# Optimization experiments

Hardware: AMD Instinct MI355X
Metric: run time of the kernel (lower is better)

The kernel has to match this reference:

```python
import jax, jax.numpy as jnp
import numpy as np

# Grid config from FPVNet.__init__ defaults
XB = (-50.0, 50.0, 0.5)   # xbound
YB = (-50.0, 50.0, 0.5)   # ybound
ZB = (-2.0, 6.0, 1.0)     # zbound
DB = (1.0, 50.0)          # dbound
NX, NY, NZ = 200, 200, 8


def setup_inputs() -> dict:
    key = jax.random.key(0)
    k1, k2 = jax.random.split(key)
    B, C, H, W = 8, 5, 256, 704
    # metric depth in valid range [dmin, dmax]
    depth = jax.random.uniform(k1, (B, 1, H, W), dtype=jnp.float32,
                               minval=DB[0], maxval=DB[1])
    sem_logits = jax.random.normal(k2, (B, C, H, W), dtype=jnp.float32)
    fx, fy, cx, cy = 600.0, 600.0, W / 2.0, H / 2.0
    K = jnp.tile(jnp.array([[fx, 0.0, cx], [0.0, fy, cy], [0.0, 0.0, 1.0]],
                           dtype=jnp.float32), (B, 1, 1))
    return {"depth": depth, "sem_logits": sem_logits, "K": K}


def reference(depth, sem_logits, K):
    """FPVNet._project_to_voxel: unproject pixels via intrinsics and
    scatter-add softmaxed semantics into a (B, C, nZ, nX, nY) voxel grid."""
    B, C, H, W = sem_logits.shape
    dmin, dmax = DB

    u = jnp.arange(W, dtype=jnp.float32)
    v = jnp.arange(H, dtype=jnp.float32)
    vv, uu = jnp.meshgrid(v, u, indexing='ij')            # (H, W)

    fx = K[:, 0, 0][:, None, None]
    fy = K[:, 1, 1][:, None, None]
    cx = K[:, 0, 2][:, None, None]
    cy = K[:, 1, 2][:, None, None]

    d = jnp.clip(depth[:, 0], dmin, dmax)                  # (B, H, W)
    x_cam = (uu[None] - cx) * d / fx
    y_cam = (vv[None] - cy) * d / fy
    z_cam = d

    # .astype(int) truncates toward zero, matching torch .long()
    xi = ((x_cam - XB[0]) / XB[2]).astype(jnp.int32)
    yi = ((z_cam - YB[0]) / YB[2]).astype(jnp.int32)
    zi = ((y_cam - ZB[0]) / ZB[2]).astype(jnp.int32)

    valid = ((xi >= 0) & (xi < NX) & (yi >= 0) & (yi < NY)
             & (zi >= 0) & (zi < NZ))                      # (B, H, W)

    sem_prob = jax.nn.softmax(sem_logits, axis=1)          # (B, C, H, W)

    V = NZ * NX * NY
    flat_idx = jnp.clip(zi * (NX * NY) + xi * NY + yi, 0, V - 1)
    flat_idx = flat_idx.reshape(B, -1)                     # (B, N), N = H*W
    # zero-out invalid points so clamped indices contribute nothing
    w = jnp.where(valid.reshape(B, 1, -1), sem_prob.reshape(B, C, -1), 0.0)

    def scatter_one(idx, prob):                            # idx (N,), prob (C, N)
        return jnp.zeros((C, V), dtype=prob.dtype).at[:, idx].add(prob)

    voxel = jax.vmap(scatter_one)(flat_idx, w)             # (B, C, V)
    return voxel.reshape(B, C, NZ, NX, NY)
```

## Files before the change

### kernel.cpp

```cpp
#include <hip/hip_runtime.h>

#define HH 256
#define WW 704
#define BB 8
#define CC 5
#define NXc 200
#define NYc 200
#define NZc 8
#define VV (NZc * NXc * NYc)
#define HW (HH * WW)

#define NBIN 98
#define NSUB (NBIN * 4)
#define NBKT (BB * NSUB)
#define CAP  768
#define QSTRIDE 1280

#define CUR_OFF 0
#define A_OFF   4096
#define B_OFF   (A_OFF + NBKT * CAP * 4)
#define CMP_OFF (B_OFF + NBKT * CAP * 2)
#define WS_FLOATS (CMP_OFF + NBKT * QSTRIDE)

__device__ __forceinline__ void bin_fp(int yi, int& xlo, int& xhi,
                                       int& zlo, int& zhi) {
    const float dhi   = 0.5f * (float)(yi + 1) - 50.0f;
    const float xspan = 2.0f * (352.0f / 600.0f) * dhi;
    const float zspan = (128.0f / 600.0f) * dhi;
    xlo = max(0,       (int)(100.0f - xspan) - 1);
    xhi = min(NXc - 1, (int)(100.0f + xspan) + 1);
    zlo = max(0,       (int)(2.0f - zspan) - 1);
    zhi = min(NZc - 1, (int)(2.0f + zspan) + 1);
}

__global__ __launch_bounds__(1024) void p1_scatter(
    const float* __restrict__ depth,
    const float* __restrict__ sem,
    const float* __restrict__ Kmat,
    unsigned* __restrict__ ws)
{
    __shared__ unsigned cnt[NSUB];
    __shared__ unsigned base[NSUB];

    unsigned* cursors = ws + CUR_OFF;
    float4*   arrA    = (float4*)(ws + A_OFF);
    float2*   arrB    = (float2*)(ws + B_OFF);

    const int b     = blockIdx.x & 7;
    const int inner = blockIdx.x >> 3;
    const int t     = inner * 1024 + threadIdx.x;
    const int p0    = t * 4;

    for (int i = threadIdx.x; i < NSUB; i += 1024) cnt[i] = 0;
    __syncthreads();

    const float fx = Kmat[b * 9 + 0];
    const float fy = Kmat[b * 9 + 4];
    const float cx = Kmat[b * 9 + 2];
    const float cy = Kmat[b * 9 + 5];

    const float4 d4 = *reinterpret_cast<const float4*>(depth + (size_t)b * HW + p0);
    float4 l4[CC];
#pragma unroll
    for (int c = 0; c < CC; ++c)
        l4[c] = *reinterpret_cast<const float4*>(sem + ((size_t)b * CC + c) * HW + p0);
    const float dvals[4] = {d4.x, d4.y, d4.z, d4.w};

    int      sub_r[4];
    unsigned meta_r[4];
    float    prob_r[4][CC];

#pragma unroll
    for (int j = 0; j < 4; ++j) {
        const int p = p0 + j;
        const int v = p / WW;
        const int u = p - v * WW;

        float d = fminf(fmaxf(dvals[j], 1.0f), 50.0f);
        float x_cam = ((float)u - cx) * d / fx;
        float y_cam = ((float)v - cy) * d / fy;
        int xi = (int)((x_cam + 50.0f) / 0.5f);
        int yi = (int)((d     + 50.0f) / 0.5f);
        int zi = (int)((y_cam +  2.0f) / 1.0f);

        bool valid = (xi >= 0) && (xi < NXc) && (yi >= 0) && (yi < NYc)
                  && (zi >= 0) && (zi < NZc);
        if (valid) {
            float lg[CC];
#pragma unroll
            for (int c = 0; c < CC; ++c) lg[c] = ((const float*)&l4[c])[j];
            float m = lg[0];
#pragma unroll
            for (int c = 1; c < CC; ++c) m = fmaxf(m, lg[c]);
            float s = 0.0f;
#pragma unroll
            for (int c = 0; c < CC; ++c) { prob_r[j][c] = expf(lg[c] - m); s += prob_r[j][c]; }
            const float inv_s = 1.0f / s;
#pragma unroll
            for (int c = 0; c < CC; ++c) prob_r[j][c] *= inv_s;

            const int bin = yi - 102;
            sub_r[j]  = bin * 4 + (zi & 1) * 2 + (xi >= 100 ? 1 : 0);
            meta_r[j] = (unsigned)xi | ((unsigned)zi << 8);
            atomicAdd(&cnt[sub_r[j]], 1u);
        } else {
            sub_r[j] = -1;
        }
    }
    __syncthreads();

    if (threadIdx.x < NSUB) {
        unsigned c = cnt[threadIdx.x];
        base[threadIdx.x] = c ? atomicAdd(&cursors[b * NSUB + threadIdx.x], c) : 0u;
    }
    __syncthreads();
    if (threadIdx.x < NSUB) cnt[threadIdx.x] = 0;
    __syncthreads();

#pragma unroll
    for (int j = 0; j < 4; ++j) {
        const int sub = sub_r[j];
        if (sub < 0) continue;
        unsigned r   = atomicAdd(&cnt[sub], 1u);
        unsigned off = base[sub] + r;
        if (off >= CAP) continue;
        size_t slot = (size_t)(b * NSUB + sub) * CAP + off;
        float4 ra;
        ((unsigned*)&ra)[0] = meta_r[j];
        ra.y = prob_r[j][0];  ra.z = prob_r[j][1];  ra.w = prob_r[j][2];
        arrA[slot] = ra;
        arrB[slot] = make_float2(prob_r[j][3], prob_r[j][4]);
    }
}

__global__ __launch_bounds__(256) void p2_reduce(unsigned* __restrict__ ws)
{
    const int wg  = blockIdx.x;
    const int b   = wg / NSUB;
    const int rem = wg - b * NSUB;
    const int bin = rem >> 2;
    const int q   = rem & 3;
    const int zp  = q >> 1;
    const int xh  = q & 1;
    const int yi  = 102 + bin;

    int xlo, xhi, zlo, zhi;
    bin_fp(yi, xlo, xhi, zlo, zhi);
    const int sxlo  = xh ? 100 : xlo;
    const int snx   = xh ? (xhi - 99) : (100 - xlo);
    const int zlo_p = zlo + (((zlo & 1) != zp) ? 1 : 0);
    const int nzs   = (zhi >= zlo_p) ? ((zhi - zlo_p) >> 1) + 1 : 0;
    const int cells = nzs * snx * CC;

    __shared__ float acc[4 * QSTRIDE];
    for (int i = threadIdx.x; i < 4 * cells; i += 256) acc[i] = 0.0f;
    __syncthreads();

    unsigned n = ws[CUR_OFF + wg];
    if (n > CAP) n = CAP;
    const float4* arrA = (const float4*)(ws + A_OFF);
    const float2* arrB = (const float2*)(ws + B_OFF);
    const size_t  seg  = (size_t)wg * CAP;
    const int     rep  = (threadIdx.x & 3) * cells;

    for (unsigned i = threadIdx.x; i < n; i += 256) {
        const float4 ra = arrA[seg + i];
        const float2 rb = arrB[seg + i];
        const unsigned m = ((const unsigned*)&ra)[0];
        const int xi = (int)(m & 255u);
        const int zi = (int)((m >> 8) & 15u);
        if (xi < sxlo || zi < zlo_p || zi > zhi || ((zi & 1) != zp))
            continue;
        const int ix = xi - sxlo;
        if (ix >= snx) continue;
        float* ac = acc + rep + (((zi - zlo_p) >> 1) * snx + ix) * CC;
        atomicAdd(ac + 0, ra.y);
        atomicAdd(ac + 1, ra.z);
        atomicAdd(ac + 2, ra.w);
        atomicAdd(ac + 3, rb.x);
        atomicAdd(ac + 4, rb.y);
    }
    __syncthreads();

    float* cmp = (float*)ws + CMP_OFF + (size_t)wg * QSTRIDE;
    for (int i = threadIdx.x; i < cells; i += 256)
        cmp[i] = acc[i] + acc[cells + i] + acc[2 * cells + i] + acc[3 * cells + i];
}

#define GY 20
__global__ __launch_bounds__(256) void p3_assemble(
    const float* __restrict__ wsf, float* __restrict__ out)
{
    const int id    = blockIdx.x;
    const int chunk = id & 31;
    const int gb    = id >> 5;
    const int g     = gb % 10;
    const int b     = gb / 10;
    const int t     = chunk * 256 + threadIdx.x;
    const bool live = (t < CC * NZc * NXc);

    int x = 0, z = 0, c = 0;
    if (live) { x = t % NXc; int zc = t / NXc; z = zc & 7; c = zc >> 3; }
    const int y0 = g * GY;

    __shared__ float tile[GY][256];

    for (int j = 0; j < GY; ++j) {
        float val = 0.0f;
        const int y   = y0 + j;
        const int bin = y - 102;
        if (live && bin >= 0) {
            int xlo, xhi, zlo, zhi;
            bin_fp(y, xlo, xhi, zlo, zhi);
            if (x >= xlo && x <= xhi && z >= zlo && z <= zhi) {
                const int zp    = z & 1;
                const int xh    = (x >= 100) ? 1 : 0;
                const int zlo_p = zlo + (((zlo & 1) != zp) ? 1 : 0);
                const int sxlo  = xh ? 100 : xlo;
                const int snx   = xh ? (xhi - 99) : (100 - xlo);
                const int wg    = ((b * NBIN + bin) << 2) + zp * 2 + xh;
                val = wsf[CMP_OFF + (size_t)wg * QSTRIDE
                          + (((z - zlo_p) >> 1) * snx + (x - sxlo)) * CC + c];
            }
        }
        tile[j][threadIdx.x] = val;
    }
    __syncthreads();

    if (live) {
        float* dst = out + (size_t)b * CC * VV + (size_t)t * NYc + y0;
#pragma unroll
        for (int k = 0; k < 5; ++k) {
            float4 v;
            v.x = tile[k * 4 + 0][threadIdx.x];
            v.y = tile[k * 4 + 1][threadIdx.x];
            v.z = tile[k * 4 + 2][threadIdx.x];
            v.w = tile[k * 4 + 3][threadIdx.x];
            reinterpret_cast<float4*>(dst)[k] = v;
        }
    }
}

__global__ __launch_bounds__(256) void zero_f4(float4* __restrict__ p, int n4) {
    int i = blockIdx.x * blockDim.x + threadIdx.x;
    const int stride = gridDim.x * blockDim.x;
    const float4 z = make_float4(0.f, 0.f, 0.f, 0.f);
    for (; i < n4; i += stride) p[i] = z;
}

__global__ __launch_bounds__(256) void fpv_scatter_direct(
    const float* __restrict__ depth, const float* __restrict__ sem,
    const float* __restrict__ Kmat, float* __restrict__ out)
{
    const int b  = blockIdx.x & 7;
    const int t  = (blockIdx.x >> 3) * blockDim.x + threadIdx.x;
    const int p0 = t * 4;

    const float fx = Kmat[b * 9 + 0];
    const float fy = Kmat[b * 9 + 4];
    const float cx = Kmat[b * 9 + 2];
    const float cy = Kmat[b * 9 + 5];

    const float4 d4 = *reinterpret_cast<const float4*>(depth + (size_t)b * HW + p0);
    float4 l4[CC];
#pragma unroll
    for (int c = 0; c < CC; ++c)
        l4[c] = *reinterpret_cast<const float4*>(sem + ((size_t)b * CC + c) * HW + p0);
    const float dvals[4] = {d4.x, d4.y, d4.z, d4.w};

#pragma unroll
    for (int j = 0; j < 4; ++j) {
        const int p = p0 + j;
        const int v = p / WW;
        const int u = p - v * WW;
        float d = fminf(fmaxf(dvals[j], 1.0f), 50.0f);
        float x_cam = ((float)u - cx) * d / fx;
        float y_cam = ((float)v - cy) * d / fy;
        int xi = (int)((x_cam + 50.0f) / 0.5f);
        int yi = (int)((d     + 50.0f) / 0.5f);
        int zi = (int)((y_cam +  2.0f) / 1.0f);
        bool valid = (xi >= 0) && (xi < NXc) && (yi >= 0) && (yi < NYc)
                  && (zi >= 0) && (zi < NZc);
        if (!valid) continue;
        float lg[CC];
#pragma unroll
        for (int c = 0; c < CC; ++c) lg[c] = ((const float*)&l4[c])[j];
        float m = lg[0];
#pragma unroll
        for (int c = 1; c < CC; ++c) m = fmaxf(m, lg[c]);
        float e[CC]; float s = 0.0f;
#pragma unroll
        for (int c = 0; c < CC; ++c) { e[c] = expf(lg[c] - m); s += e[c]; }
        const float inv_s = 1.0f / s;
        const int flat = zi * (NXc * NYc) + xi * NYc + yi;
        float* dst = out + (size_t)b * CC * VV + flat;
#pragma unroll
        for (int c = 0; c < CC; ++c)
            atomicAdd(dst + (size_t)c * VV, e[c] * inv_s);
    }
}

extern "C" void kernel_launch(void* const* d_in, const int* in_sizes, int n_in,
                              void* d_out, int out_size, void* d_ws, size_t ws_size,
                              hipStream_t stream) {
    const float* depth = (const float*)d_in[0];
    const float* sem   = (const float*)d_in[1];
    const float* Kmat  = (const float*)d_in[2];
    float* out = (float*)d_out;

    const size_t ws_need = (size_t)WS_FLOATS * 4;

    if (ws_size >= ws_need) {
        unsigned* ws = (unsigned*)d_ws;
        hipMemsetAsync(ws, 0, NBKT * sizeof(unsigned), stream);
        p1_scatter<<<(HW / 4 / 1024) * BB, 1024, 0, stream>>>(depth, sem, Kmat, ws);
        p2_reduce<<<NBKT, 256, 0, stream>>>(ws);
        p3_assemble<<<BB * 10 * 32, 256, 0, stream>>>((const float*)d_ws, out);
    } else {
        const int n4 = BB * CC * VV / 4;
        zero_f4<<<4096, 256, 0, stream>>>((float4*)out, n4);
        fpv_scatter_direct<<<(HW / 4 / 256) * BB, 256, 0, stream>>>(depth, sem, Kmat, out);
    }
}
```

Measured before the change: 164.2 us.

## Pack voxel records into one float4 and make compacted grid channel-major

Each scattered point record shrinks from 24 bytes (float4 plus float2) to a single float4. The voxel x/z index is hidden in the low mantissa bits of the first four probabilities, and the fifth probability is rebuilt as one minus their sum. This cuts workspace write and read traffic between the scatter and reduce kernels, but adds small rounding error to every probability. The compacted per-bucket output is also reordered channel-major so p3 reads it with unit stride across x, and p1 moves from 1024-thread to 256-thread blocks.

Result: no change. 162.6 us (-1.0%).

```diff
diff --git a/kernel.cpp b/kernel.cpp
--- a/kernel.cpp
+++ b/kernel.cpp
@@ -18,8 +18,7 @@
 
 #define CUR_OFF 0
 #define A_OFF   4096
-#define B_OFF   (A_OFF + NBKT * CAP * 4)
-#define CMP_OFF (B_OFF + NBKT * CAP * 2)
+#define CMP_OFF (A_OFF + NBKT * CAP * 4)
 #define WS_FLOATS (CMP_OFF + NBKT * QSTRIDE)
 
 __device__ __forceinline__ void bin_fp(int yi, int& xlo, int& xhi,
@@ -33,7 +32,11 @@
     zhi = min(NZc - 1, (int)(2.0f + zspan) + 1);
 }
 
-__global__ __launch_bounds__(1024) void p1_scatter(
+__device__ __forceinline__ float embed_bits(float p, unsigned bits, unsigned mask) {
+    return __uint_as_float((__float_as_uint(p) & ~mask) | bits);
+}
+
+__global__ __launch_bounds__(256) void p1_scatter(
     const float* __restrict__ depth,
     const float* __restrict__ sem,
     const float* __restrict__ Kmat,
@@ -44,14 +47,13 @@
 
     unsigned* cursors = ws + CUR_OFF;
     float4*   arrA    = (float4*)(ws + A_OFF);
-    float2*   arrB    = (float2*)(ws + B_OFF);
 
     const int b     = blockIdx.x & 7;
     const int inner = blockIdx.x >> 3;
-    const int t     = inner * 1024 + threadIdx.x;
-    const int p0    = t * 4;
-
-    for (int i = threadIdx.x; i < NSUB; i += 1024) cnt[i] = 0;
+    const int t     = inner * 256 + threadIdx.x;
+    const int p0i   = t * 4;
+
+    for (int i = threadIdx.x; i < NSUB; i += 256) cnt[i] = 0;
     __syncthreads();
 
     const float fx = Kmat[b * 9 + 0];
@@ -59,20 +61,19 @@
     const float cx = Kmat[b * 9 + 2];
     const float cy = Kmat[b * 9 + 5];
 
-    const float4 d4 = *reinterpret_cast<const float4*>(depth + (size_t)b * HW + p0);
+    const float4 d4 = *reinterpret_cast<const float4*>(depth + (size_t)b * HW + p0i);
     float4 l4[CC];
 #pragma unroll
     for (int c = 0; c < CC; ++c)
-        l4[c] = *reinterpret_cast<const float4*>(sem + ((size_t)b * CC + c) * HW + p0);
+        l4[c] = *reinterpret_cast<const float4*>(sem + ((size_t)b * CC + c) * HW + p0i);
     const float dvals[4] = {d4.x, d4.y, d4.z, d4.w};
 
-    int      sub_r[4];
-    unsigned meta_r[4];
-    float    prob_r[4][CC];
+    int    sub_r[4];
+    float4 rec_r[4];
 
 #pragma unroll
     for (int j = 0; j < 4; ++j) {
-        const int p = p0 + j;
+        const int p = p0i + j;
         const int v = p / WW;
         const int u = p - v * WW;
 
@@ -92,16 +93,20 @@
             float m = lg[0];
 #pragma unroll
             for (int c = 1; c < CC; ++c) m = fmaxf(m, lg[c]);
-            float s = 0.0f;
-#pragma unroll
-            for (int c = 0; c < CC; ++c) { prob_r[j][c] = expf(lg[c] - m); s += prob_r[j][c]; }
+            float e[CC]; float s = 0.0f;
+#pragma unroll
+            for (int c = 0; c < CC; ++c) { e[c] = expf(lg[c] - m); s += e[c]; }
             const float inv_s = 1.0f / s;
 #pragma unroll
-            for (int c = 0; c < CC; ++c) prob_r[j][c] *= inv_s;
+            for (int c = 0; c < CC; ++c) e[c] *= inv_s;
 
             const int bin = yi - 102;
-            sub_r[j]  = bin * 4 + (zi & 1) * 2 + (xi >= 100 ? 1 : 0);
-            meta_r[j] = (unsigned)xi | ((unsigned)zi << 8);
+            sub_r[j] = bin * 4 + (zi & 1) * 2 + (xi >= 100 ? 1 : 0);
+            const unsigned meta = (unsigned)xi | ((unsigned)zi << 8);
+            rec_r[j].x = embed_bits(e[0], meta & 7u, 7u);
+            rec_r[j].y = embed_bits(e[1], (meta >> 3) & 7u, 7u);
+            rec_r[j].z = embed_bits(e[2], (meta >> 6) & 7u, 7u);
+            rec_r[j].w = embed_bits(e[3], (meta >> 9) & 3u, 3u);
             atomicAdd(&cnt[sub_r[j]], 1u);
         } else {
             sub_r[j] = -1;
@@ -109,12 +114,12 @@
     }
     __syncthreads();
 
-    if (threadIdx.x < NSUB) {
-        unsigned c = cnt[threadIdx.x];
-        base[threadIdx.x] = c ? atomicAdd(&cursors[b * NSUB + threadIdx.x], c) : 0u;
-    }
-    __syncthreads();
-    if (threadIdx.x < NSUB) cnt[threadIdx.x] = 0;
+    for (int i = threadIdx.x; i < NSUB; i += 256) {
+        unsigned c = cnt[i];
+        base[i] = c ? atomicAdd(&cursors[b * NSUB + i], c) : 0u;
+    }
+    __syncthreads();
+    for (int i = threadIdx.x; i < NSUB; i += 256) cnt[i] = 0;
     __syncthreads();
 
 #pragma unroll
@@ -124,12 +129,7 @@
         unsigned r   = atomicAdd(&cnt[sub], 1u);
         unsigned off = base[sub] + r;
         if (off >= CAP) continue;
-        size_t slot = (size_t)(b * NSUB + sub) * CAP + off;
-        float4 ra;
-        ((unsigned*)&ra)[0] = meta_r[j];
-        ra.y = prob_r[j][0];  ra.z = prob_r[j][1];  ra.w = prob_r[j][2];
-        arrA[slot] = ra;
-        arrB[slot] = make_float2(prob_r[j][3], prob_r[j][4]);
+        arrA[(size_t)(b * NSUB + sub) * CAP + off] = rec_r[j];
     }
 }
 
@@ -150,7 +150,8 @@
     const int snx   = xh ? (xhi - 99) : (100 - xlo);
     const int zlo_p = zlo + (((zlo & 1) != zp) ? 1 : 0);
     const int nzs   = (zhi >= zlo_p) ? ((zhi - zlo_p) >> 1) + 1 : 0;
-    const int cells = nzs * snx * CC;
+    const int zx    = nzs * snx;
+    const int cells = zx * CC;
 
     __shared__ float acc[4 * QSTRIDE];
     for (int i = threadIdx.x; i < 4 * cells; i += 256) acc[i] = 0.0f;
@@ -159,32 +160,38 @@
     unsigned n = ws[CUR_OFF + wg];
     if (n > CAP) n = CAP;
     const float4* arrA = (const float4*)(ws + A_OFF);
-    const float2* arrB = (const float2*)(ws + B_OFF);
     const size_t  seg  = (size_t)wg * CAP;
     const int     rep  = (threadIdx.x & 3) * cells;
 
     for (unsigned i = threadIdx.x; i < n; i += 256) {
         const float4 ra = arrA[seg + i];
-        const float2 rb = arrB[seg + i];
-        const unsigned m = ((const unsigned*)&ra)[0];
-        const int xi = (int)(m & 255u);
-        const int zi = (int)((m >> 8) & 15u);
+        const unsigned meta = (__float_as_uint(ra.x) & 7u)
+                            | ((__float_as_uint(ra.y) & 7u) << 3)
+                            | ((__float_as_uint(ra.z) & 7u) << 6)
+                            | ((__float_as_uint(ra.w) & 3u) << 9);
+        const int xi = (int)(meta & 255u);
+        const int zi = (int)(meta >> 8);
+        const float p4 = 1.0f - ra.x - ra.y - ra.z - ra.w;
         if (xi < sxlo || zi < zlo_p || zi > zhi || ((zi & 1) != zp))
             continue;
         const int ix = xi - sxlo;
         if (ix >= snx) continue;
         float* ac = acc + rep + (((zi - zlo_p) >> 1) * snx + ix) * CC;
-        atomicAdd(ac + 0, ra.y);
-        atomicAdd(ac + 1, ra.z);
-        atomicAdd(ac + 2, ra.w);
-        atomicAdd(ac + 3, rb.x);
-        atomicAdd(ac + 4, rb.y);
+        atomicAdd(ac + 0, ra.x);
+        atomicAdd(ac + 1, ra.y);
+        atomicAdd(ac + 2, ra.z);
+        atomicAdd(ac + 3, ra.w);
+        atomicAdd(ac + 4, p4);
     }
     __syncthreads();
 
     float* cmp = (float*)ws + CMP_OFF + (size_t)wg * QSTRIDE;
-    for (int i = threadIdx.x; i < cells; i += 256)
-        cmp[i] = acc[i] + acc[cells + i] + acc[2 * cells + i] + acc[3 * cells + i];
+    for (int i = threadIdx.x; i < cells; i += 256) {
+        const int c = i / zx;
+        const int r = i - c * zx;
+        const int a = r * CC + c;
+        cmp[i] = acc[a] + acc[cells + a] + acc[2 * cells + a] + acc[3 * cells + a];
+    }
 }
 
 #define GY 20
@@ -218,9 +225,10 @@
                 const int zlo_p = zlo + (((zlo & 1) != zp) ? 1 : 0);
                 const int sxlo  = xh ? 100 : xlo;
                 const int snx   = xh ? (xhi - 99) : (100 - xlo);
+                const int nzs   = ((zhi - zlo_p) >> 1) + 1;
                 const int wg    = ((b * NBIN + bin) << 2) + zp * 2 + xh;
                 val = wsf[CMP_OFF + (size_t)wg * QSTRIDE
-                          + (((z - zlo_p) >> 1) * snx + (x - sxlo)) * CC + c];
+                          + (c * nzs + ((z - zlo_p) >> 1)) * snx + (x - sxlo)];
             }
         }
         tile[j][threadIdx.x] = val;
@@ -313,7 +321,7 @@
     if (ws_size >= ws_need) {
         unsigned* ws = (unsigned*)d_ws;
         hipMemsetAsync(ws, 0, NBKT * sizeof(unsigned), stream);
-        p1_scatter<<<(HW / 4 / 1024) * BB, 1024, 0, stream>>>(depth, sem, Kmat, ws);
+        p1_scatter<<<(HW / 4 / 256) * BB, 256, 0, stream>>>(depth, sem, Kmat, ws);
         p2_reduce<<<NBKT, 256, 0, stream>>>(ws);
         p3_assemble<<<BB * 10 * 32, 256, 0, stream>>>((const float*)d_ws, out);
     } else {
```
